# Kernel tuning notes

Hardware: AMD Instinct MI355X
Metric: run time of the kernel (lower is better)

Reference implementation:

```python
import jax, jax.numpy as jnp
import numpy as np

NEG_SLOPE = 0.2
CONV3_NUM, CONV1_NUM, POLY_NUM = 3, 5, 4
FEAT_DIM = CONV3_NUM * 84 + CONV1_NUM * 12 + POLY_NUM * 12  # 360
DN = ('NCHW', 'OIHW', 'NCHW')


def leaky_relu(x):
    return jnp.where(x >= 0, x, NEG_SLOPE * x)


def conv3x3(x, feat):
    # per-sample dynamic 3x3 conv: feat[:, :81] -> kernel [3,3,3,3], feat[:, 81:84] -> bias
    B = x.shape[0]
    k = feat[:, :81].reshape(B, 3, 3, 3, 3)
    b = feat[:, 81:84]

    def one(xi, ki, bi):
        y = jax.lax.conv_general_dilated(xi[None], ki, (1, 1), 'SAME', dimension_numbers=DN)[0]
        return y + bi[:, None, None]

    return leaky_relu(jax.vmap(one)(x, k, b))


def conv1x1(x, feat):
    B = x.shape[0]
    k = feat[:, :9].reshape(B, 3, 3, 1, 1)
    b = feat[:, 9:12]

    def one(xi, ki, bi):
        y = jax.lax.conv_general_dilated(xi[None], ki, (1, 1), 'VALID', dimension_numbers=DN)[0]
        return y + bi[:, None, None]

    return leaky_relu(jax.vmap(one)(x, k, b))


def conv_stack(x, feature):
    residual = x
    for i in range(CONV3_NUM):
        x = conv3x3(x, feature[:, i * 84:(i + 1) * 84])
    off = CONV3_NUM * 84
    for i in range(CONV1_NUM):
        x = conv1x1(x, feature[:, off + i * 12:off + (i + 1) * 12])
    return residual + x


def att_map(feat, h_mat, w_mat, xc):
    # product over POLY_NUM of (a*h + b*w + c*x + d)
    att = jnp.ones_like(xc)
    for i in range(POLY_NUM):
        a = feat[:, i * 4 + 0].reshape(-1, 1, 1, 1)
        b = feat[:, i * 4 + 1].reshape(-1, 1, 1, 1)
        c = feat[:, i * 4 + 2].reshape(-1, 1, 1, 1)
        d = feat[:, i * 4 + 3].reshape(-1, 1, 1, 1)
        att = att * (a * h_mat + b * w_mat + c * xc + d)
    return att


def apply_attention(x, feature):
    H, W = x.shape[2], x.shape[3]
    h_mat = (jnp.arange(H, dtype=x.dtype) / H).reshape(1, 1, H, 1)
    w_mat = (jnp.arange(W, dtype=x.dtype) / W).reshape(1, 1, 1, W)
    off = CONV3_NUM * 84 + CONV1_NUM * 12
    atts = [att_map(feature[:, off + c * POLY_NUM * 4: off + (c + 1) * POLY_NUM * 4],
                    h_mat, w_mat, x[:, c:c + 1]) for c in range(3)]  # R, G, B
    att = jnp.concatenate(atts, axis=1)
    return x * (1 + att)


def setup_inputs() -> dict:
    key = jax.random.key(0)
    k1, k2, k3 = jax.random.split(key, 3)
    x = jax.random.uniform(k1, (8, 3, 512, 512), dtype=jnp.float32)
    thumb_x = jax.random.uniform(k2, (8, 3, 64, 64), dtype=jnp.float32)
    Wm = jax.random.normal(k3, (3, FEAT_DIM), dtype=jnp.float32) * 0.05
    bm = jnp.zeros((FEAT_DIM,), dtype=jnp.float32)
    return {"x": x, "thumb_x": thumb_x, "Wm": Wm, "bm": bm}


def reference(x, thumb_x, Wm, bm):
    # meta: GAP over thumbnail -> linear -> per-sample hypernetwork features [B, 360]
    feature = jnp.mean(thumb_x, axis=(2, 3)) @ Wm + bm
    x = conv_stack(x, feature)
    x = apply_attention(x, feature)
    thumb = conv_stack(thumb_x, feature)
    thumb = apply_attention(thumb, feature)
    return (x, thumb)
```

## Files before the change

kernel.cpp:

```cpp
#include <hip/hip_runtime.h>


#define LEAKY(v) fmaxf((v), 0.2f * (v))

constexpr int STRD = 72;
constexpr int CHS  = 38 * 72;
constexpr int BUFSZ = 3 * CHS + 16;

__global__ __launch_bounds__(256) void means_kernel(
    const float* __restrict__ thumb, float* __restrict__ ws)
{
    const int bc = blockIdx.x;
    const int tid = threadIdx.x;
    const float4* p = (const float4*)(thumb + (size_t)bc * 4096);
    float s = 0.f;
#pragma unroll
    for (int k = 0; k < 4; ++k) {
        float4 v = p[tid + k * 256];
        s += v.x + v.y + v.z + v.w;
    }
    __shared__ float red[256];
    red[tid] = s;
    __syncthreads();
    for (int off = 128; off > 0; off >>= 1) {
        if (tid < off) red[tid] += red[tid + off];
        __syncthreads();
    }
    if (tid == 0) ws[bc] = red[0] * (1.f / 4096.f);
}

__global__ __launch_bounds__(384) void fmm_kernel(
    const float* __restrict__ Wm, const float* __restrict__ bm,
    const float* __restrict__ ws, float* __restrict__ feat)
{
    const int b = blockIdx.x;
    const int f = threadIdx.x;
    if (f < 360) {
        const float m0 = ws[b * 3 + 0], m1 = ws[b * 3 + 1], m2 = ws[b * 3 + 2];
        feat[b * 360 + f] =
            fmaf(m0, Wm[f], fmaf(m1, Wm[360 + f], fmaf(m2, Wm[720 + f], bm[f])));
    }
}

template<int R, bool CLAMPROW>
__device__ __forceinline__ void conv_rows(
    const float* __restrict__ buf, const float* __restrict__ fw,
    int r0, int gx, float4 acc[][3])
{
    const float b0 = fw[81], b1 = fw[82], b2 = fw[83];
#pragma unroll
    for (int j = 0; j < R; ++j) {
        acc[j][0] = make_float4(b0, b0, b0, b0);
        acc[j][1] = make_float4(b1, b1, b1, b1);
        acc[j][2] = make_float4(b2, b2, b2, b2);
    }
    const int gA = (gx < 0) ? 0 : gx;
#pragma unroll
    for (int ich = 0; ich < 3; ++ich) {
#pragma unroll
        for (int ri = 0; ri < R + 2; ++ri) {
            int mr = r0 - 1 + ri + 3;
            if (CLAMPROW) mr = (mr > 37) ? 37 : mr;
            const int idx = ich * CHS + mr * STRD;
            const float4 A = *(const float4*)&buf[idx + gA];
            const float4 B = *(const float4*)&buf[idx + gx + 4];
            const float4 C = *(const float4*)&buf[idx + gx + 8];
#pragma unroll
            for (int j = 0; j < R; ++j) {
                const int dy = ri - j;
                if (dy < 0 || dy > 2) continue;
#pragma unroll
                for (int oc = 0; oc < 3; ++oc) {
                    const float w0 = fw[oc * 27 + ich * 9 + dy * 3 + 0];
                    const float w1 = fw[oc * 27 + ich * 9 + dy * 3 + 1];
                    const float w2 = fw[oc * 27 + ich * 9 + dy * 3 + 2];
                    float4& a = acc[j][oc];
                    a.x = fmaf(A.w, w0, fmaf(B.x, w1, fmaf(B.y, w2, a.x)));
                    a.y = fmaf(B.x, w0, fmaf(B.y, w1, fmaf(B.z, w2, a.y)));
                    a.z = fmaf(B.y, w0, fmaf(B.z, w1, fmaf(B.w, w2, a.z)));
                    a.w = fmaf(B.z, w0, fmaf(B.w, w1, fmaf(C.x, w2, a.w)));
                }
            }
        }
    }
}

__global__ __launch_bounds__(256, 2) void conv_att_kernel(
    const float* __restrict__ x, const float* __restrict__ thumb,
    const float* __restrict__ feat, float* __restrict__ out)
{
    __shared__ float buf[BUFSZ];

    int id = blockIdx.x;
    const float* src; float* dst; int H, W, b, trow, tcol;
    if (id < 1024) {
        b = id >> 7; const int t = id & 127;
        H = 512; W = 512; trow = (t >> 3) * 32; tcol = (t & 7) * 64;
        src = x; dst = out;
    } else {
        const int i2 = id - 1024;
        b = i2 >> 1; trow = (i2 & 1) * 32; tcol = 0;
        H = 64; W = 64; src = thumb;
        dst = out + (size_t)8 * 3 * 512 * 512;
    }
    const float* fb = feat + b * 360;
    const int tid = threadIdx.x;

    const float* sbg = src + (size_t)b * 3 * H * W;
    for (int q = tid; q < 2052; q += 256) {
        const int c = q / 684;
        const int rem = q - c * 684;
        const int mr = rem / 18;
        const int mq = rem - mr * 18;
        const int gr = trow + mr - 3;
        const int gc0 = tcol + 4 * mq - 4;
        const bool rok = (unsigned)gr < (unsigned)H;
        const float* gp = sbg + (size_t)c * H * W + (size_t)(rok ? gr : 0) * W;
        float4 v;
        if (rok && (unsigned)gc0 <= (unsigned)(W - 4)) {
            v = *(const float4*)&gp[gc0];
        } else {
            v.x = (rok && (unsigned)(gc0 + 0) < (unsigned)W) ? gp[gc0 + 0] : 0.f;
            v.y = (rok && (unsigned)(gc0 + 1) < (unsigned)W) ? gp[gc0 + 1] : 0.f;
            v.z = (rok && (unsigned)(gc0 + 2) < (unsigned)W) ? gp[gc0 + 2] : 0.f;
            v.w = (rok && (unsigned)(gc0 + 3) < (unsigned)W) ? gp[gc0 + 3] : 0.f;
        }
        *(float4*)&buf[c * CHS + mr * STRD + 4 * mq] = v;
    }
    __syncthreads();

    const int s3 = tid >> 4;
    const int gx3 = 4 * (tid & 15);

    const bool act12 = tid < 216;
    const int s12 = tid / 18;
    const int g12 = tid - s12 * 18;
    const int gx12 = 4 * g12 - 4;
    float4 acc[3][3];
    if (act12) conv_rows<3, false>(buf, fb, 3 * s12 - 2, gx12, acc);

    float4 res[2][3];
#pragma unroll
    for (int j = 0; j < 2; ++j)
#pragma unroll
        for (int c = 0; c < 3; ++c)
            res[j][c] = *(const float4*)&buf[c * CHS + (2 * s3 + j + 3) * STRD + gx3 + 4];
    __syncthreads();

    if (act12) {
        const int r0 = 3 * s12 - 2;
#pragma unroll
        for (int j = 0; j < 3; ++j)
#pragma unroll
            for (int oc = 0; oc < 3; ++oc) {
                float4 v = acc[j][oc];
                v.x = LEAKY(v.x); v.y = LEAKY(v.y); v.z = LEAKY(v.z); v.w = LEAKY(v.w);
                *(float4*)&buf[oc * CHS + (r0 + j + 3) * STRD + gx12 + 4] = v;
            }
    }
    __syncthreads();

    if (act12) conv_rows<3, true>(buf, fb + 84, 3 * s12 - 1, gx12, acc);
    __syncthreads();

    if (act12) {
        const int r0 = 3 * s12 - 1;
#pragma unroll
        for (int j = 0; j < 3; ++j) {
            if (r0 + j > 32) continue;
#pragma unroll
            for (int oc = 0; oc < 3; ++oc) {
                float4 v = acc[j][oc];
                v.x = LEAKY(v.x); v.y = LEAKY(v.y); v.z = LEAKY(v.z); v.w = LEAKY(v.w);
                *(float4*)&buf[oc * CHS + (r0 + j + 3) * STRD + gx12 + 4] = v;
            }
        }
    }
    __syncthreads();

    float4 y[2][3];
    conv_rows<2, false>(buf, fb + 168, 2 * s3, gx3, y);
#pragma unroll
    for (int j = 0; j < 2; ++j)
#pragma unroll
        for (int oc = 0; oc < 3; ++oc) {
            y[j][oc].x = LEAKY(y[j][oc].x); y[j][oc].y = LEAKY(y[j][oc].y);
            y[j][oc].z = LEAKY(y[j][oc].z); y[j][oc].w = LEAKY(y[j][oc].w);
        }

#pragma unroll
    for (int lay = 0; lay < 5; ++lay) {
        const float* fw = fb + 252 + lay * 12;
        const float w00 = fw[0], w01 = fw[1], w02 = fw[2];
        const float w10 = fw[3], w11 = fw[4], w12 = fw[5];
        const float w20 = fw[6], w21 = fw[7], w22 = fw[8];
        const float c0 = fw[9], c1 = fw[10], c2 = fw[11];
#pragma unroll
        for (int j = 0; j < 2; ++j) {
            float4 z0, z1, z2;
            z0.x = fmaf(y[j][0].x, w00, fmaf(y[j][1].x, w01, fmaf(y[j][2].x, w02, c0)));
            z0.y = fmaf(y[j][0].y, w00, fmaf(y[j][1].y, w01, fmaf(y[j][2].y, w02, c0)));
            z0.z = fmaf(y[j][0].z, w00, fmaf(y[j][1].z, w01, fmaf(y[j][2].z, w02, c0)));
            z0.w = fmaf(y[j][0].w, w00, fmaf(y[j][1].w, w01, fmaf(y[j][2].w, w02, c0)));
            z1.x = fmaf(y[j][0].x, w10, fmaf(y[j][1].x, w11, fmaf(y[j][2].x, w12, c1)));
            z1.y = fmaf(y[j][0].y, w10, fmaf(y[j][1].y, w11, fmaf(y[j][2].y, w12, c1)));
            z1.z = fmaf(y[j][0].z, w10, fmaf(y[j][1].z, w11, fmaf(y[j][2].z, w12, c1)));
            z1.w = fmaf(y[j][0].w, w10, fmaf(y[j][1].w, w11, fmaf(y[j][2].w, w12, c1)));
            z2.x = fmaf(y[j][0].x, w20, fmaf(y[j][1].x, w21, fmaf(y[j][2].x, w22, c2)));
            z2.y = fmaf(y[j][0].y, w20, fmaf(y[j][1].y, w21, fmaf(y[j][2].y, w22, c2)));
            z2.z = fmaf(y[j][0].z, w20, fmaf(y[j][1].z, w21, fmaf(y[j][2].z, w22, c2)));
            z2.w = fmaf(y[j][0].w, w20, fmaf(y[j][1].w, w21, fmaf(y[j][2].w, w22, c2)));
            y[j][0].x = LEAKY(z0.x); y[j][0].y = LEAKY(z0.y); y[j][0].z = LEAKY(z0.z); y[j][0].w = LEAKY(z0.w);
            y[j][1].x = LEAKY(z1.x); y[j][1].y = LEAKY(z1.y); y[j][1].z = LEAKY(z1.z); y[j][1].w = LEAKY(z1.w);
            y[j][2].x = LEAKY(z2.x); y[j][2].y = LEAKY(z2.y); y[j][2].z = LEAKY(z2.z); y[j][2].w = LEAKY(z2.w);
        }
    }

    const float invH = 1.f / (float)H;
    const float invW = 1.f / (float)W;
    const float wbase = (float)(tcol + gx3) * invW;
    const float4 wv = make_float4(wbase, wbase + invW, wbase + 2.f * invW, wbase + 3.f * invW);
#pragma unroll
    for (int ch = 0; ch < 3; ++ch) {
        const float* fp = fb + 312 + ch * 16;
        const float pa0 = fp[0], pb0 = fp[1], pc0 = fp[2], pd0 = fp[3];
        const float pa1 = fp[4], pb1 = fp[5], pc1 = fp[6], pd1 = fp[7];
        const float pa2 = fp[8], pb2 = fp[9], pc2 = fp[10], pd2 = fp[11];
        const float pa3 = fp[12], pb3 = fp[13], pc3 = fp[14], pd3 = fp[15];
#pragma unroll
        for (int j = 0; j < 2; ++j) {
            const int gr = trow + 2 * s3 + j;
            const float h = (float)gr * invH;
            float4 v;
            v.x = y[j][ch].x + res[j][ch].x;
            v.y = y[j][ch].y + res[j][ch].y;
            v.z = y[j][ch].z + res[j][ch].z;
            v.w = y[j][ch].w + res[j][ch].w;
            const float t0 = fmaf(pa0, h, pd0), t1 = fmaf(pa1, h, pd1);
            const float t2 = fmaf(pa2, h, pd2), t3 = fmaf(pa3, h, pd3);
            float4 o;
            {
                float a0 = fmaf(pb0, wv.x, fmaf(pc0, v.x, t0));
                a0 *= fmaf(pb1, wv.x, fmaf(pc1, v.x, t1));
                a0 *= fmaf(pb2, wv.x, fmaf(pc2, v.x, t2));
                a0 *= fmaf(pb3, wv.x, fmaf(pc3, v.x, t3));
                o.x = v.x * (1.f + a0);
                float a1 = fmaf(pb0, wv.y, fmaf(pc0, v.y, t0));
                a1 *= fmaf(pb1, wv.y, fmaf(pc1, v.y, t1));
                a1 *= fmaf(pb2, wv.y, fmaf(pc2, v.y, t2));
                a1 *= fmaf(pb3, wv.y, fmaf(pc3, v.y, t3));
                o.y = v.y * (1.f + a1);
                float a2 = fmaf(pb0, wv.z, fmaf(pc0, v.z, t0));
                a2 *= fmaf(pb1, wv.z, fmaf(pc1, v.z, t1));
                a2 *= fmaf(pb2, wv.z, fmaf(pc2, v.z, t2));
                a2 *= fmaf(pb3, wv.z, fmaf(pc3, v.z, t3));
                o.z = v.z * (1.f + a2);
                float a3 = fmaf(pb0, wv.w, fmaf(pc0, v.w, t0));
                a3 *= fmaf(pb1, wv.w, fmaf(pc1, v.w, t1));
                a3 *= fmaf(pb2, wv.w, fmaf(pc2, v.w, t2));
                a3 *= fmaf(pb3, wv.w, fmaf(pc3, v.w, t3));
                o.w = v.w * (1.f + a3);
            }
            *(float4*)&dst[((size_t)(b * 3 + ch) * H + gr) * W + tcol + gx3] = o;
        }
    }
}

extern "C" void kernel_launch(void* const* d_in, const int* in_sizes, int n_in,
                              void* d_out, int out_size, void* d_ws, size_t ws_size,
                              hipStream_t stream) {
    const float* x = (const float*)d_in[0];
    const float* thumb = (const float*)d_in[1];
    const float* Wm = (const float*)d_in[2];
    const float* bm = (const float*)d_in[3];
    float* out = (float*)d_out;
    float* means = (float*)d_ws;
    float* feat = (float*)d_ws + 64;

    means_kernel<<<24, 256, 0, stream>>>(thumb, means);
    fmm_kernel<<<8, 384, 0, stream>>>(Wm, bm, means, feat);
    conv_att_kernel<<<1040, 256, 0, stream>>>(x, thumb, feat, out);
}
```

Before: 124.8 us.

## Halve conv tile height to 16 rows and fuse mean/feature kernels

Shrinks each block's output tile from 32x64 to 16x64. That cuts shared memory from 38 to 22 staged rows per channel, so each block needs much less LDS and the grid doubles to 2080 blocks, which should raise occupancy and make load balancing finer. Each thread now computes one output row instead of two, and the conv stages are reworked with 2-row accumulators. It also fuses the thumbnail-mean and feature matmul into a single kernel, removing one launch. The trade-off is a larger halo overhead: 6 halo rows per 16-row tile instead of per 32, which means more redundant global loads and recomputed 3x3 conv work.

```diff
diff --git a/kernel.cpp b/kernel.cpp
--- a/kernel.cpp
+++ b/kernel.cpp
@@ -4,45 +4,43 @@
 #define LEAKY(v) fmaxf((v), 0.2f * (v))
 
 constexpr int STRD = 72;
-constexpr int CHS  = 38 * 72;
+constexpr int ROWS0 = 22;
+constexpr int CHS  = ROWS0 * STRD;
 constexpr int BUFSZ = 3 * CHS + 16;
 
-__global__ __launch_bounds__(256) void means_kernel(
-    const float* __restrict__ thumb, float* __restrict__ ws)
-{
-    const int bc = blockIdx.x;
-    const int tid = threadIdx.x;
-    const float4* p = (const float4*)(thumb + (size_t)bc * 4096);
-    float s = 0.f;
-#pragma unroll
-    for (int k = 0; k < 4; ++k) {
-        float4 v = p[tid + k * 256];
-        s += v.x + v.y + v.z + v.w;
-    }
-    __shared__ float red[256];
-    red[tid] = s;
-    __syncthreads();
-    for (int off = 128; off > 0; off >>= 1) {
-        if (tid < off) red[tid] += red[tid + off];
-        __syncthreads();
-    }
-    if (tid == 0) ws[bc] = red[0] * (1.f / 4096.f);
-}
-
-__global__ __launch_bounds__(384) void fmm_kernel(
-    const float* __restrict__ Wm, const float* __restrict__ bm,
-    const float* __restrict__ ws, float* __restrict__ feat)
+__global__ __launch_bounds__(256) void feat_kernel(
+    const float* __restrict__ thumb, const float* __restrict__ Wm,
+    const float* __restrict__ bm, float* __restrict__ feat)
 {
     const int b = blockIdx.x;
-    const int f = threadIdx.x;
-    if (f < 360) {
-        const float m0 = ws[b * 3 + 0], m1 = ws[b * 3 + 1], m2 = ws[b * 3 + 2];
+    const int tid = threadIdx.x;
+    __shared__ float red[256];
+    __shared__ float smean[3];
+
+    for (int c = 0; c < 3; ++c) {
+        const float4* p = (const float4*)(thumb + (size_t)(b * 3 + c) * 4096);
+        float s = 0.f;
+#pragma unroll
+        for (int k = 0; k < 4; ++k) {
+            float4 v = p[tid + k * 256];
+            s += v.x + v.y + v.z + v.w;
+        }
+        red[tid] = s;
+        __syncthreads();
+        for (int off = 128; off > 0; off >>= 1) {
+            if (tid < off) red[tid] += red[tid + off];
+            __syncthreads();
+        }
+        if (tid == 0) smean[c] = red[0] * (1.f / 4096.f);
+        __syncthreads();
+    }
+    const float m0 = smean[0], m1 = smean[1], m2 = smean[2];
+    for (int f = tid; f < 360; f += 256)
         feat[b * 360 + f] =
             fmaf(m0, Wm[f], fmaf(m1, Wm[360 + f], fmaf(m2, Wm[720 + f], bm[f])));
-    }
-}
-
-template<int R, bool CLAMPROW>
+}
+
+template<int R>
 __device__ __forceinline__ void conv_rows(
     const float* __restrict__ buf, const float* __restrict__ fw,
     int r0, int gx, float4 acc[][3])
@@ -59,8 +57,7 @@
     for (int ich = 0; ich < 3; ++ich) {
 #pragma unroll
         for (int ri = 0; ri < R + 2; ++ri) {
-            int mr = r0 - 1 + ri + 3;
-            if (CLAMPROW) mr = (mr > 37) ? 37 : mr;
+            const int mr = r0 + 2 + ri;
             const int idx = ich * CHS + mr * STRD;
             const float4 A = *(const float4*)&buf[idx + gA];
             const float4 B = *(const float4*)&buf[idx + gx + 4];
@@ -93,13 +90,13 @@
 
     int id = blockIdx.x;
     const float* src; float* dst; int H, W, b, trow, tcol;
-    if (id < 1024) {
-        b = id >> 7; const int t = id & 127;
-        H = 512; W = 512; trow = (t >> 3) * 32; tcol = (t & 7) * 64;
+    if (id < 2048) {
+        b = id >> 8; const int t = id & 255;
+        H = 512; W = 512; trow = (t >> 3) * 16; tcol = (t & 7) * 64;
         src = x; dst = out;
     } else {
-        const int i2 = id - 1024;
-        b = i2 >> 1; trow = (i2 & 1) * 32; tcol = 0;
+        const int i2 = id - 2048;
+        b = i2 >> 2; trow = (i2 & 3) * 16; tcol = 0;
         H = 64; W = 64; src = thumb;
         dst = out + (size_t)8 * 3 * 512 * 512;
     }
@@ -107,9 +104,9 @@
     const int tid = threadIdx.x;
 
     const float* sbg = src + (size_t)b * 3 * H * W;
-    for (int q = tid; q < 2052; q += 256) {
-        const int c = q / 684;
-        const int rem = q - c * 684;
+    for (int q = tid; q < 1188; q += 256) {
+        const int c = q / 396;
+        const int rem = q - c * 396;
         const int mr = rem / 18;
         const int mq = rem - mr * 18;
         const int gr = trow + mr - 3;
@@ -132,61 +129,56 @@
     const int s3 = tid >> 4;
     const int gx3 = 4 * (tid & 15);
 
-    const bool act12 = tid < 216;
-    const int s12 = tid / 18;
-    const int g12 = tid - s12 * 18;
-    const int gx12 = 4 * g12 - 4;
-    float4 acc[3][3];
-    if (act12) conv_rows<3, false>(buf, fb, 3 * s12 - 2, gx12, acc);
-
-    float4 res[2][3];
-#pragma unroll
-    for (int j = 0; j < 2; ++j)
-#pragma unroll
-        for (int c = 0; c < 3; ++c)
-            res[j][c] = *(const float4*)&buf[c * CHS + (2 * s3 + j + 3) * STRD + gx3 + 4];
-    __syncthreads();
-
-    if (act12) {
-        const int r0 = 3 * s12 - 2;
-#pragma unroll
-        for (int j = 0; j < 3; ++j)
+    const bool act1 = tid < 180;
+    const int s1 = tid / 18;
+    const int gx1 = 4 * (tid - s1 * 18) - 4;
+    float4 acc[2][3];
+    if (act1) conv_rows<2>(buf, fb, 2 * s1 - 2, gx1, acc);
+
+    float4 res[3];
+#pragma unroll
+    for (int c = 0; c < 3; ++c)
+        res[c] = *(const float4*)&buf[c * CHS + (s3 + 3) * STRD + gx3 + 4];
+    __syncthreads();
+
+    if (act1) {
+        const int r0 = 2 * s1 - 2;
+#pragma unroll
+        for (int j = 0; j < 2; ++j)
 #pragma unroll
             for (int oc = 0; oc < 3; ++oc) {
                 float4 v = acc[j][oc];
                 v.x = LEAKY(v.x); v.y = LEAKY(v.y); v.z = LEAKY(v.z); v.w = LEAKY(v.w);
-                *(float4*)&buf[oc * CHS + (r0 + j + 3) * STRD + gx12 + 4] = v;
+                *(float4*)&buf[oc * CHS + (r0 + j + 3) * STRD + gx1 + 4] = v;
             }
     }
     __syncthreads();
 
-    if (act12) conv_rows<3, true>(buf, fb + 84, 3 * s12 - 1, gx12, acc);
-    __syncthreads();
-
-    if (act12) {
-        const int r0 = 3 * s12 - 1;
-#pragma unroll
-        for (int j = 0; j < 3; ++j) {
-            if (r0 + j > 32) continue;
+    const bool act2 = tid < 162;
+    const int s2 = tid / 18;
+    const int gx2 = 4 * (tid - s2 * 18) - 4;
+    if (act2) conv_rows<2>(buf, fb + 84, 2 * s2 - 1, gx2, acc);
+    __syncthreads();
+
+    if (act2) {
+        const int r0 = 2 * s2 - 1;
+#pragma unroll
+        for (int j = 0; j < 2; ++j)
 #pragma unroll
             for (int oc = 0; oc < 3; ++oc) {
                 float4 v = acc[j][oc];
                 v.x = LEAKY(v.x); v.y = LEAKY(v.y); v.z = LEAKY(v.z); v.w = LEAKY(v.w);
-                *(float4*)&buf[oc * CHS + (r0 + j + 3) * STRD + gx12 + 4] = v;
+                *(float4*)&buf[oc * CHS + (r0 + j + 3) * STRD + gx2 + 4] = v;
             }
-        }
-    }
-    __syncthreads();
-
-    float4 y[2][3];
-    conv_rows<2, false>(buf, fb + 168, 2 * s3, gx3, y);
-#pragma unroll
-    for (int j = 0; j < 2; ++j)
-#pragma unroll
-        for (int oc = 0; oc < 3; ++oc) {
-            y[j][oc].x = LEAKY(y[j][oc].x); y[j][oc].y = LEAKY(y[j][oc].y);
-            y[j][oc].z = LEAKY(y[j][oc].z); y[j][oc].w = LEAKY(y[j][oc].w);
-        }
+    }
+    __syncthreads();
+
+    float4 y[1][3];
+    conv_rows<1>(buf, fb + 168, s3, gx3, y);
+    float4 y0 = y[0][0], y1 = y[0][1], y2 = y[0][2];
+    y0.x = LEAKY(y0.x); y0.y = LEAKY(y0.y); y0.z = LEAKY(y0.z); y0.w = LEAKY(y0.w);
+    y1.x = LEAKY(y1.x); y1.y = LEAKY(y1.y); y1.z = LEAKY(y1.z); y1.w = LEAKY(y1.w);
+    y2.x = LEAKY(y2.x); y2.y = LEAKY(y2.y); y2.z = LEAKY(y2.z); y2.w = LEAKY(y2.w);
 
 #pragma unroll
     for (int lay = 0; lay < 5; ++lay) {
@@ -195,29 +187,28 @@
         const float w10 = fw[3], w11 = fw[4], w12 = fw[5];
         const float w20 = fw[6], w21 = fw[7], w22 = fw[8];
         const float c0 = fw[9], c1 = fw[10], c2 = fw[11];
-#pragma unroll
-        for (int j = 0; j < 2; ++j) {
-            float4 z0, z1, z2;
-            z0.x = fmaf(y[j][0].x, w00, fmaf(y[j][1].x, w01, fmaf(y[j][2].x, w02, c0)));
-            z0.y = fmaf(y[j][0].y, w00, fmaf(y[j][1].y, w01, fmaf(y[j][2].y, w02, c0)));
-            z0.z = fmaf(y[j][0].z, w00, fmaf(y[j][1].z, w01, fmaf(y[j][2].z, w02, c0)));
-            z0.w = fmaf(y[j][0].w, w00, fmaf(y[j][1].w, w01, fmaf(y[j][2].w, w02, c0)));
-            z1.x = fmaf(y[j][0].x, w10, fmaf(y[j][1].x, w11, fmaf(y[j][2].x, w12, c1)));
-            z1.y = fmaf(y[j][0].y, w10, fmaf(y[j][1].y, w11, fmaf(y[j][2].y, w12, c1)));
-            z1.z = fmaf(y[j][0].z, w10, fmaf(y[j][1].z, w11, fmaf(y[j][2].z, w12, c1)));
-            z1.w = fmaf(y[j][0].w, w10, fmaf(y[j][1].w, w11, fmaf(y[j][2].w, w12, c1)));
-            z2.x = fmaf(y[j][0].x, w20, fmaf(y[j][1].x, w21, fmaf(y[j][2].x, w22, c2)));
-            z2.y = fmaf(y[j][0].y, w20, fmaf(y[j][1].y, w21, fmaf(y[j][2].y, w22, c2)));
-            z2.z = fmaf(y[j][0].z, w20, fmaf(y[j][1].z, w21, fmaf(y[j][2].z, w22, c2)));
-            z2.w = fmaf(y[j][0].w, w20, fmaf(y[j][1].w, w21, fmaf(y[j][2].w, w22, c2)));
-            y[j][0].x = LEAKY(z0.x); y[j][0].y = LEAKY(z0.y); y[j][0].z = LEAKY(z0.z); y[j][0].w = LEAKY(z0.w);
-            y[j][1].x = LEAKY(z1.x); y[j][1].y = LEAKY(z1.y); y[j][1].z = LEAKY(z1.z); y[j][1].w = LEAKY(z1.w);
-            y[j][2].x = LEAKY(z2.x); y[j][2].y = LEAKY(z2.y); y[j][2].z = LEAKY(z2.z); y[j][2].w = LEAKY(z2.w);
-        }
+        float4 z0, z1, z2;
+        z0.x = fmaf(y0.x, w00, fmaf(y1.x, w01, fmaf(y2.x, w02, c0)));
+        z0.y = fmaf(y0.y, w00, fmaf(y1.y, w01, fmaf(y2.y, w02, c0)));
+        z0.z = fmaf(y0.z, w00, fmaf(y1.z, w01, fmaf(y2.z, w02, c0)));
+        z0.w = fmaf(y0.w, w00, fmaf(y1.w, w01, fmaf(y2.w, w02, c0)));
+        z1.x = fmaf(y0.x, w10, fmaf(y1.x, w11, fmaf(y2.x, w12, c1)));
+        z1.y = fmaf(y0.y, w10, fmaf(y1.y, w11, fmaf(y2.y, w12, c1)));
+        z1.z = fmaf(y0.z, w10, fmaf(y1.z, w11, fmaf(y2.z, w12, c1)));
+        z1.w = fmaf(y0.w, w10, fmaf(y1.w, w11, fmaf(y2.w, w12, c1)));
+        z2.x = fmaf(y0.x, w20, fmaf(y1.x, w21, fmaf(y2.x, w22, c2)));
+        z2.y = fmaf(y0.y, w20, fmaf(y1.y, w21, fmaf(y2.y, w22, c2)));
+        z2.z = fmaf(y0.z, w20, fmaf(y1.z, w21, fmaf(y2.z, w22, c2)));
+        z2.w = fmaf(y0.w, w20, fmaf(y1.w, w21, fmaf(y2.w, w22, c2)));
+        y0.x = LEAKY(z0.x); y0.y = LEAKY(z0.y); y0.z = LEAKY(z0.z); y0.w = LEAKY(z0.w);
+        y1.x = LEAKY(z1.x); y1.y = LEAKY(z1.y); y1.z = LEAKY(z1.z); y1.w = LEAKY(z1.w);
+        y2.x = LEAKY(z2.x); y2.y = LEAKY(z2.y); y2.z = LEAKY(z2.z); y2.w = LEAKY(z2.w);
     }
 
     const float invH = 1.f / (float)H;
     const float invW = 1.f / (float)W;
+    const int gr = trow + s3;
+    const float h = (float)gr * invH;
     const float wbase = (float)(tcol + gx3) * invW;
     const float4 wv = make_float4(wbase, wbase + invW, wbase + 2.f * invW, wbase + 3.f * invW);
 #pragma unroll
@@ -227,42 +218,36 @@
         const float pa1 = fp[4], pb1 = fp[5], pc1 = fp[6], pd1 = fp[7];
         const float pa2 = fp[8], pb2 = fp[9], pc2 = fp[10], pd2 = fp[11];
         const float pa3 = fp[12], pb3 = fp[13], pc3 = fp[14], pd3 = fp[15];
-#pragma unroll
-        for (int j = 0; j < 2; ++j) {
-            const int gr = trow + 2 * s3 + j;
-            const float h = (float)gr * invH;
-            float4 v;
-            v.x = y[j][ch].x + res[j][ch].x;
-            v.y = y[j][ch].y + res[j][ch].y;
-            v.z = y[j][ch].z + res[j][ch].z;
-            v.w = y[j][ch].w + res[j][ch].w;
-            const float t0 = fmaf(pa0, h, pd0), t1 = fmaf(pa1, h, pd1);
-            const float t2 = fmaf(pa2, h, pd2), t3 = fmaf(pa3, h, pd3);
-            float4 o;
-            {
-                float a0 = fmaf(pb0, wv.x, fmaf(pc0, v.x, t0));
-                a0 *= fmaf(pb1, wv.x, fmaf(pc1, v.x, t1));
-                a0 *= fmaf(pb2, wv.x, fmaf(pc2, v.x, t2));
-                a0 *= fmaf(pb3, wv.x, fmaf(pc3, v.x, t3));
-                o.x = v.x * (1.f + a0);
-                float a1 = fmaf(pb0, wv.y, fmaf(pc0, v.y, t0));
-                a1 *= fmaf(pb1, wv.y, fmaf(pc1, v.y, t1));
-                a1 *= fmaf(pb2, wv.y, fmaf(pc2, v.y, t2));
-                a1 *= fmaf(pb3, wv.y, fmaf(pc3, v.y, t3));
-                o.y = v.y * (1.f + a1);
-                float a2 = fmaf(pb0, wv.z, fmaf(pc0, v.z, t0));
-                a2 *= fmaf(pb1, wv.z, fmaf(pc1, v.z, t1));
-                a2 *= fmaf(pb2, wv.z, fmaf(pc2, v.z, t2));
-                a2 *= fmaf(pb3, wv.z, fmaf(pc3, v.z, t3));
-                o.z = v.z * (1.f + a2);
-                float a3 = fmaf(pb0, wv.w, fmaf(pc0, v.w, t0));
-                a3 *= fmaf(pb1, wv.w, fmaf(pc1, v.w, t1));
-                a3 *= fmaf(pb2, wv.w, fmaf(pc2, v.w, t2));
-                a3 *= fmaf(pb3, wv.w, fmaf(pc3, v.w, t3));
-                o.w = v.w * (1.f + a3);
-            }
-            *(float4*)&dst[((size_t)(b * 3 + ch) * H + gr) * W + tcol + gx3] = o;
-        }
+        const float4 yv = (ch == 0) ? y0 : (ch == 1) ? y1 : y2;
+        float4 v;
+        v.x = yv.x + res[ch].x;
+        v.y = yv.y + res[ch].y;
+        v.z = yv.z + res[ch].z;
+        v.w = yv.w + res[ch].w;
+        const float t0 = fmaf(pa0, h, pd0), t1 = fmaf(pa1, h, pd1);
+        const float t2 = fmaf(pa2, h, pd2), t3 = fmaf(pa3, h, pd3);
+        float4 o;
+        float a0 = fmaf(pb0, wv.x, fmaf(pc0, v.x, t0));
+        a0 *= fmaf(pb1, wv.x, fmaf(pc1, v.x, t1));
+        a0 *= fmaf(pb2, wv.x, fmaf(pc2, v.x, t2));
+        a0 *= fmaf(pb3, wv.x, fmaf(pc3, v.x, t3));
+        o.x = v.x * (1.f + a0);
+        float a1 = fmaf(pb0, wv.y, fmaf(pc0, v.y, t0));
+        a1 *= fmaf(pb1, wv.y, fmaf(pc1, v.y, t1));
+        a1 *= fmaf(pb2, wv.y, fmaf(pc2, v.y, t2));
+        a1 *= fmaf(pb3, wv.y, fmaf(pc3, v.y, t3));
+        o.y = v.y * (1.f + a1);
+        float a2 = fmaf(pb0, wv.z, fmaf(pc0, v.z, t0));
+        a2 *= fmaf(pb1, wv.z, fmaf(pc1, v.z, t1));
+        a2 *= fmaf(pb2, wv.z, fmaf(pc2, v.z, t2));
+        a2 *= fmaf(pb3, wv.z, fmaf(pc3, v.z, t3));
+        o.z = v.z * (1.f + a2);
+        float a3 = fmaf(pb0, wv.w, fmaf(pc0, v.w, t0));
+        a3 *= fmaf(pb1, wv.w, fmaf(pc1, v.w, t1));
+        a3 *= fmaf(pb2, wv.w, fmaf(pc2, v.w, t2));
+        a3 *= fmaf(pb3, wv.w, fmaf(pc3, v.w, t3));
+        o.w = v.w * (1.f + a3);
+        *(float4*)&dst[((size_t)(b * 3 + ch) * H + gr) * W + tcol + gx3] = o;
     }
 }
 
@@ -274,10 +259,8 @@
     const float* Wm = (const float*)d_in[2];
     const float* bm = (const float*)d_in[3];
     float* out = (float*)d_out;
-    float* means = (float*)d_ws;
-    float* feat = (float*)d_ws + 64;
-
-    means_kernel<<<24, 256, 0, stream>>>(thumb, means);
-    fmm_kernel<<<8, 384, 0, stream>>>(Wm, bm, means, feat);
-    conv_att_kernel<<<1040, 256, 0, stream>>>(x, thumb, feat, out);
-}
+    float* feat = (float*)d_ws;
+
+    feat_kernel<<<8, 256, 0, stream>>>(thumb, Wm, bm, feat);
+    conv_att_kernel<<<2080, 256, 0, stream>>>(x, thumb, feat, out);
+}
```

Result: faster. 120.4 us (-3.5%).
